# Kernel tuning notes

Hardware: AMD Instinct MI355X
Metric: run time of the kernel (lower is better)

## Reference

```python
import jax, jax.numpy as jnp
import numpy as np

N = 100000       # nodes
E = 3200000      # directed edges (avg_degree ~32)
F_IN = 512
H = 16
C = 7


def setup_inputs() -> dict:
    key = jax.random.key(0)
    k1, k2, k3, k4 = jax.random.split(key, 4)
    x = jax.random.normal(k1, (N, F_IN), dtype=jnp.float32)
    edge_index = jax.random.randint(k2, (2, E), 0, N, dtype=jnp.int32)
    # Glorot-ish init for weights
    W1 = jax.random.normal(k3, (F_IN, H), dtype=jnp.float32) * (1.0 / np.sqrt(F_IN))
    b1 = jnp.zeros((H,), dtype=jnp.float32)
    W2 = jax.random.normal(k4, (H, C), dtype=jnp.float32) * (1.0 / np.sqrt(H))
    b2 = jnp.zeros((C,), dtype=jnp.float32)
    return {"x": x, "edge_index": edge_index, "W1": W1, "b1": b1, "W2": W2, "b2": b2}


def _gcn_prep(edge_index, n):
    # add self-loops (PyG GCNConv default: add_self_loops=True)
    loop = jnp.arange(n, dtype=edge_index.dtype)
    src = jnp.concatenate([edge_index[0], loop])  # [E+N]
    dst = jnp.concatenate([edge_index[1], loop])  # [E+N]
    # symmetric normalization deg^{-1/2} (A+I) deg^{-1/2}; deg over targets
    deg = jax.ops.segment_sum(jnp.ones_like(dst, dtype=jnp.float32), dst, num_segments=n)
    dinv = jax.lax.rsqrt(jnp.maximum(deg, 1.0))  # deg >= 1 due to self-loops
    norm = dinv[src] * dinv[dst]                 # [E+N]
    return src, dst, norm


def _gcn_conv(h, src, dst, norm, W, b, n):
    h = h @ W                                            # [N, out] transform first (small out dim)
    msg = h[src] * norm[:, None]                         # gather + scale, [E+N, out]
    out = jax.ops.segment_sum(msg, dst, num_segments=n)  # scatter-add
    return out + b


def reference(x, edge_index, W1, b1, W2, b2):
    n = x.shape[0]
    src, dst, norm = _gcn_prep(edge_index, n)
    h = _gcn_conv(x, src, dst, norm, W1, b1, n)
    h = jax.nn.relu(h)
    # F.dropout(training=self.training) is identity in eval mode
    h = _gcn_conv(h, src, dst, norm, W2, b2, n)
    return jax.nn.log_softmax(h, axis=1)
```

## Files before the change

### kernel.cpp

```cpp
#include <hip/hip_runtime.h>
#include <math.h>

#define F_IN 512
#define H1 16
#define C_OUT 7
#define BSHIFT 8
#define BNODES 256
#define SRCMASK 0x1FFFFu
#define P3CAP 8960
#define BCAP 8960

__device__ __forceinline__ unsigned bf16pair(float a, float b) {
    unsigned ua = __float_as_uint(a);
    unsigned ub = __float_as_uint(b);
    ua = (ua + 0x7FFFu + ((ua >> 16) & 1u)) >> 16;
    ub = (ub + 0x7FFFu + ((ub >> 16) & 1u)) & 0xFFFF0000u;
    return ua | ub;
}

__global__ __launch_bounds__(1024) void k_zero(int* __restrict__ cur, int B) {
    int t = threadIdx.x;
    if (t < B) cur[t] = 0;
}

__global__ __launch_bounds__(1024) void k_fill_p2(
    const int* __restrict__ src, const int* __restrict__ dst,
    int* __restrict__ cur, unsigned* __restrict__ bedge, int E, int B) {
    __shared__ int lh[1024];
    __shared__ int scan[1024];
    __shared__ int gb[1024];
    __shared__ unsigned lsort[4096];
    __shared__ unsigned short lbk[4096];
    int t = threadIdx.x;
    for (int i = t; i < B; i += 1024) lh[i] = 0;
    __syncthreads();
    int e0 = blockIdx.x * 4096;
    int myb[4], myr[4];
    unsigned myv[4];
#pragma unroll
    for (int k = 0; k < 4; k++) {
        int e = e0 + t + 1024 * k;
        myb[k] = -1;
        if (e < E) {
            int d = dst[e];
            int b = d >> BSHIFT;
            myb[k] = b;
            myv[k] = ((unsigned)(d & (BNODES - 1)) << 17) | (unsigned)src[e];
            myr[k] = atomicAdd(&lh[b], 1);
        }
    }
    __syncthreads();
    int v = (t < B) ? lh[t] : 0;
    scan[t] = v;
    __syncthreads();
    for (int off = 1; off < 1024; off <<= 1) {
        int x = (t >= off) ? scan[t - off] : 0;
        __syncthreads();
        scan[t] += x;
        __syncthreads();
    }
    scan[t] -= v;
    __syncthreads();
    if (t < B && v > 0) gb[t] = t * BCAP + atomicAdd(&cur[t], v);
    __syncthreads();
#pragma unroll
    for (int k = 0; k < 4; k++) {
        if (myb[k] >= 0) {
            int slot = scan[myb[k]] + myr[k];
            lsort[slot] = myv[k];
            lbk[slot] = (unsigned short)myb[k];
        }
    }
    __syncthreads();
    int elim = min(4096, E - e0);
    for (int i = t; i < elim; i += 1024) {
        int b = lbk[i];
        int idx = gb[b] + (i - scan[b]);
        if (idx < (b + 1) * BCAP) bedge[idx] = lsort[i];
    }
}

__global__ __launch_bounds__(256) void k_fill_p3(
    const int* __restrict__ cur, const unsigned* __restrict__ bedge,
    int* __restrict__ csr_src, int* __restrict__ indeg, int* __restrict__ rowptr,
    float* __restrict__ dinv, int n) {
    __shared__ int lh[BNODES];
    __shared__ int off[BNODES];
    __shared__ int lc[BNODES];
    __shared__ int sc[BNODES];
    __shared__ int lsort[P3CAP];
    int t = threadIdx.x;
    int bb = blockIdx.x;
    int nodebase = bb << BSHIFT;
    int gs = bb * BCAP;
    int ge = gs + min(cur[bb], BCAP);
    for (int i = t; i < BNODES; i += 256) { lh[i] = 0; lc[i] = 0; }
    __syncthreads();
    for (int e = gs + t; e < ge; e += 256) {
        unsigned v = bedge[e];
        atomicAdd(&lh[v >> 17], 1);
    }
    __syncthreads();
    int sv = (t < BNODES) ? lh[t] : 0;
    if (t < BNODES) sc[t] = sv;
    __syncthreads();
    for (int o = 1; o < BNODES; o <<= 1) {
        int x = (t < BNODES && t >= o) ? sc[t - o] : 0;
        __syncthreads();
        if (t < BNODES) sc[t] += x;
        __syncthreads();
    }
    if (t < BNODES) off[t] = sc[t] - sv;
    __syncthreads();
    if (t < BNODES) {
        int node = nodebase + t;
        if (node < n) {
            indeg[node] = sv;
            rowptr[node] = gs + off[t];
            dinv[node] = rsqrtf(1.0f + (float)sv);
        }
    }
    for (int e = gs + t; e < ge; e += 256) {
        unsigned v = bedge[e];
        int dl = (int)(v >> 17);
        int rank = atomicAdd(&lc[dl], 1);
        int pos = off[dl] + rank;
        int svv = (int)(v & SRCMASK);
        if (pos < P3CAP) lsort[pos] = svv;
        else csr_src[gs + pos] = svv;
    }
    __syncthreads();
    int lim = min(ge - gs, P3CAP);
    for (int i = t; i < lim; i += 256) csr_src[gs + i] = lsort[i];
}

template<int KH>
__device__ __forceinline__ void gemm1_half(const float* __restrict__ xs,
                                           const float* __restrict__ W1,
                                           int kc, int lrow, float* __restrict__ acc) {
#pragma unroll 4
    for (int k = 0; k < 32; k++) {
        float xv = xs[(KH + k) * 129 + lrow];
        const float* w = W1 + (kc + KH + k) * H1;
#pragma unroll
        for (int c = 0; c < H1; c++) acc[c] = fmaf(xv, w[c], acc[c]);
    }
}

__global__ __launch_bounds__(256) void k_gemm1(
    const float* __restrict__ x, const float* __restrict__ W1,
    const float* __restrict__ dinv, unsigned short* __restrict__ g1, int n) {
    __shared__ float xs[64 * 129];
    const int t = threadIdx.x;
    const int rowbase = blockIdx.x * 128;
    const int lrow = t & 127;
    const int kh = t >> 7;

    float acc[H1];
#pragma unroll
    for (int c = 0; c < H1; c++) acc[c] = 0.0f;

    for (int kc = 0; kc < F_IN; kc += 64) {
        __syncthreads();
#pragma unroll
        for (int jj = 0; jj < 8; jj++) {
            int f = t + 256 * jj;
            int r = f >> 4;
            int kq = f & 15;
            int grow = rowbase + r;
            float4 v = *(const float4*)(x + (size_t)min(grow, n - 1) * F_IN + kc + kq * 4);
            xs[(kq * 4 + 0) * 129 + r] = v.x;
            xs[(kq * 4 + 1) * 129 + r] = v.y;
            xs[(kq * 4 + 2) * 129 + r] = v.z;
            xs[(kq * 4 + 3) * 129 + r] = v.w;
        }
        __syncthreads();
        if (kh == 0) gemm1_half<0>(xs, W1, kc, lrow, acc);
        else         gemm1_half<32>(xs, W1, kc, lrow, acc);
    }
    __syncthreads();
    float* red = xs;
    if (kh == 1) {
#pragma unroll
        for (int c = 0; c < H1; c++) red[lrow * H1 + c] = acc[c];
    }
    __syncthreads();
    if (kh == 0) {
        int grow = rowbase + lrow;
        if (grow < n) {
            float d = dinv[grow];
            float o[H1];
#pragma unroll
            for (int c = 0; c < H1; c++) o[c] = (acc[c] + red[lrow * H1 + c]) * d;
            unsigned pk[8];
#pragma unroll
            for (int k = 0; k < 8; k++) pk[k] = bf16pair(o[2 * k], o[2 * k + 1]);
            unsigned* gp = (unsigned*)(g1 + (size_t)grow * H1);
            *(uint4*)(gp)     = make_uint4(pk[0], pk[1], pk[2], pk[3]);
            *(uint4*)(gp + 4) = make_uint4(pk[4], pk[5], pk[6], pk[7]);
        }
    }
}

__global__ __launch_bounds__(256) void k_agg1(
    const int* __restrict__ rowptr, const int* __restrict__ indeg,
    const int* __restrict__ csr_src, const unsigned short* __restrict__ g1,
    const float* __restrict__ dinv, const float* __restrict__ b1,
    const float* __restrict__ W2, float* __restrict__ g2, int n) {
    int t = threadIdx.x;
    int node = blockIdx.x * 16 + (t >> 4);
    int l = t & 15;
    int eo = l >> 2;
    int c4 = l & 3;
    if (node >= n) return;

    float w[4][C_OUT];
#pragma unroll
    for (int kk = 0; kk < 4; kk++)
#pragma unroll
        for (int c = 0; c < C_OUT; c++)
            w[kk][c] = W2[(c4 * 4 + kk) * C_OUT + c];
    float4 b1c = *(const float4*)(b1 + c4 * 4);

    int start = rowptr[node];
    int end = start + indeg[node];
    float d = dinv[node];

    float4 s = make_float4(0.f, 0.f, 0.f, 0.f);
    if (eo == 0) {
        uint2 u = *(const uint2*)(g1 + (size_t)node * H1 + c4 * 4);
        s.x = __uint_as_float(u.x << 16);
        s.y = __uint_as_float(u.x & 0xFFFF0000u);
        s.z = __uint_as_float(u.y << 16);
        s.w = __uint_as_float(u.y & 0xFFFF0000u);
    }

    int i = start + eo;
    for (; i + 4 < end; i += 8) {
        int a0 = csr_src[i];
        int a1 = csr_src[i + 4];
        uint2 u0 = *(const uint2*)(g1 + (size_t)a0 * H1 + c4 * 4);
        uint2 u1 = *(const uint2*)(g1 + (size_t)a1 * H1 + c4 * 4);
        s.x += __uint_as_float(u0.x << 16)        + __uint_as_float(u1.x << 16);
        s.y += __uint_as_float(u0.x & 0xFFFF0000u) + __uint_as_float(u1.x & 0xFFFF0000u);
        s.z += __uint_as_float(u0.y << 16)        + __uint_as_float(u1.y << 16);
        s.w += __uint_as_float(u0.y & 0xFFFF0000u) + __uint_as_float(u1.y & 0xFFFF0000u);
    }
    if (i < end) {
        int a = csr_src[i];
        uint2 u = *(const uint2*)(g1 + (size_t)a * H1 + c4 * 4);
        s.x += __uint_as_float(u.x << 16);
        s.y += __uint_as_float(u.x & 0xFFFF0000u);
        s.z += __uint_as_float(u.y << 16);
        s.w += __uint_as_float(u.y & 0xFFFF0000u);
    }

    s.x += __shfl_xor(s.x, 4); s.y += __shfl_xor(s.y, 4);
    s.z += __shfl_xor(s.z, 4); s.w += __shfl_xor(s.w, 4);
    s.x += __shfl_xor(s.x, 8); s.y += __shfl_xor(s.y, 8);
    s.z += __shfl_xor(s.z, 8); s.w += __shfl_xor(s.w, 8);

    float4 r;
    r.x = fmaxf(fmaf(d, s.x, b1c.x), 0.f);
    r.y = fmaxf(fmaf(d, s.y, b1c.y), 0.f);
    r.z = fmaxf(fmaf(d, s.z, b1c.z), 0.f);
    r.w = fmaxf(fmaf(d, s.w, b1c.w), 0.f);

    float p[C_OUT];
#pragma unroll
    for (int c = 0; c < C_OUT; c++) {
        p[c] = r.x * w[0][c];
        p[c] = fmaf(r.y, w[1][c], p[c]);
        p[c] = fmaf(r.z, w[2][c], p[c]);
        p[c] = fmaf(r.w, w[3][c], p[c]);
    }
#pragma unroll
    for (int c = 0; c < C_OUT; c++) {
        p[c] += __shfl_xor(p[c], 1);
        p[c] += __shfl_xor(p[c], 2);
    }

    if (eo == 0 && c4 == 0) {
        float4 o = make_float4(d * p[0], d * p[1], d * p[2], d * p[3]);
        *(float4*)(g2 + (size_t)node * 8) = o;
    }
    if (eo == 0 && c4 == 1) {
        float4 o = make_float4(d * p[4], d * p[5], d * p[6], 0.0f);
        *(float4*)(g2 + (size_t)node * 8 + 4) = o;
    }
}

__global__ __launch_bounds__(256) void k_agg2(
    const int* __restrict__ rowptr, const int* __restrict__ indeg,
    const int* __restrict__ csr_src, const float* __restrict__ g2,
    const float* __restrict__ dinv, const float* __restrict__ b2,
    float* __restrict__ out, int n) {
    __shared__ float ls[32 * C_OUT];
    int t = threadIdx.x;
    int g = t >> 3;
    int node = blockIdx.x * 32 + g;
    int l = t & 7;
    int eo = l >> 1;
    int ch = l & 1;

    float4 s = make_float4(0.f, 0.f, 0.f, 0.f);
    float d = 0.f;
    bool valid = node < n;
    if (valid) {
        int start = rowptr[node];
        int end = start + indeg[node];
        d = dinv[node];
        if (eo == 0) s = *(const float4*)(g2 + (size_t)node * 8 + ch * 4);
        int i = start + eo;
        for (; i + 4 < end; i += 8) {
            int a0 = csr_src[i];
            int a1 = csr_src[i + 4];
            float4 v0 = *(const float4*)(g2 + (size_t)a0 * 8 + ch * 4);
            float4 v1 = *(const float4*)(g2 + (size_t)a1 * 8 + ch * 4);
            s.x += v0.x + v1.x;
            s.y += v0.y + v1.y;
            s.z += v0.z + v1.z;
            s.w += v0.w + v1.w;
        }
        if (i < end) {
            int a = csr_src[i];
            float4 v = *(const float4*)(g2 + (size_t)a * 8 + ch * 4);
            s.x += v.x; s.y += v.y; s.z += v.z; s.w += v.w;
        }
    }
    s.x += __shfl_xor(s.x, 2); s.y += __shfl_xor(s.y, 2);
    s.z += __shfl_xor(s.z, 2); s.w += __shfl_xor(s.w, 2);
    s.x += __shfl_xor(s.x, 4); s.y += __shfl_xor(s.y, 4);
    s.z += __shfl_xor(s.z, 4); s.w += __shfl_xor(s.w, 4);

    float4 val;
    if (ch == 0) {
        float4 bb = *(const float4*)b2;
        val.x = fmaf(d, s.x, bb.x);
        val.y = fmaf(d, s.y, bb.y);
        val.z = fmaf(d, s.z, bb.z);
        val.w = fmaf(d, s.w, bb.w);
    } else {
        val.x = fmaf(d, s.x, b2[4]);
        val.y = fmaf(d, s.y, b2[5]);
        val.z = fmaf(d, s.z, b2[6]);
        val.w = 0.f;
    }
    float m = fmaxf(fmaxf(val.x, val.y), val.z);
    if (ch == 0) m = fmaxf(m, val.w);
    m = fmaxf(m, __shfl_xor(m, 1));
    float e0 = expf(val.x - m), e1 = expf(val.y - m), e2 = expf(val.z - m);
    float e3 = (ch == 0) ? expf(val.w - m) : 0.f;
    float se = (e0 + e1) + (e2 + e3);
    se += __shfl_xor(se, 1);
    float lg = logf(se) + m;

    if (valid && eo == 0) {
        float* o = ls + g * C_OUT + ch * 4;
        o[0] = val.x - lg;
        o[1] = val.y - lg;
        o[2] = val.z - lg;
        if (ch == 0) o[3] = val.w - lg;
    }
    __syncthreads();
    int nbase = blockIdx.x * 32;
    int nv = (n - nbase < 32 ? n - nbase : 32) * C_OUT;
    if (t < nv) out[(size_t)nbase * C_OUT + t] = ls[t];
}

extern "C" void kernel_launch(void* const* d_in, const int* in_sizes, int n_in,
                              void* d_out, int out_size, void* d_ws, size_t ws_size,
                              hipStream_t stream) {
    const float* x  = (const float*)d_in[0];
    const int* ei   = (const int*)d_in[1];
    const float* W1 = (const float*)d_in[2];
    const float* b1 = (const float*)d_in[3];
    const float* W2 = (const float*)d_in[4];
    const float* b2 = (const float*)d_in[5];
    float* out = (float*)d_out;

    const int n = in_sizes[0] / F_IN;
    const int E = in_sizes[1] / 2;
    const int* src = ei;
    const int* dst = ei + E;

    const int B   = (n + BNODES - 1) >> BSHIFT;
    const int nfb = (E + 4095) >> 12;

    int*   indeg    = (int*)d_ws;
    int*   rowptr   = indeg + n;
    float* dinv     = (float*)(rowptr + n);
    int*   cur      = (int*)(dinv + n);
    unsigned short* g1 = (unsigned short*)(cur + 1024);
    float* g2       = (float*)(g1 + (size_t)n * H1);
    unsigned* bedge = (unsigned*)(g2 + (size_t)8 * n);
    int*   csr_src  = (int*)(bedge + (size_t)B * BCAP);

    k_zero<<<1, 1024, 0, stream>>>(cur, B);
    k_fill_p2<<<nfb, 1024, 0, stream>>>(src, dst, cur, bedge, E, B);
    k_fill_p3<<<B, 256, 0, stream>>>(cur, bedge, csr_src, indeg, rowptr, dinv, n);

    k_gemm1<<<(n + 127) / 128, 256, 0, stream>>>(x, W1, dinv, g1, n);
    k_agg1<<<(n + 15) / 16, 256, 0, stream>>>(rowptr, indeg, csr_src, g1, dinv, b1, W2, g2, n);
    k_agg2<<<(n + 31) / 32, 256, 0, stream>>>(rowptr, indeg, csr_src, g2, dinv, b2, out, n);
}
```

Before: 414.4 us.

## Merge CSR build stages with degree histogram and GEMM via block-range dispatch

Degrees are now computed with global atomics by extra blocks in the bucket-fill kernel. The CSR sort stage and the first-layer GEMM are merged into one launch that splits work by block index, so the GEMM no longer waits for the sort to finish. The zero kernel is replaced by a memset, and the GEMM computes dinv itself from indeg. This removes two launches and serialization between independent stages, at the cost of 3.2M extra global atomics on indeg and a larger shared-memory footprint for the sort blocks.

```diff
diff --git a/kernel.cpp b/kernel.cpp
--- a/kernel.cpp
+++ b/kernel.cpp
@@ -18,20 +18,25 @@
     return ua | ub;
 }
 
-__global__ __launch_bounds__(1024) void k_zero(int* __restrict__ cur, int B) {
-    int t = threadIdx.x;
-    if (t < B) cur[t] = 0;
-}
-
-__global__ __launch_bounds__(1024) void k_fill_p2(
+__global__ __launch_bounds__(1024) void k_p2hist(
     const int* __restrict__ src, const int* __restrict__ dst,
-    int* __restrict__ cur, unsigned* __restrict__ bedge, int E, int B) {
+    int* __restrict__ cur, unsigned* __restrict__ bedge,
+    int* __restrict__ indeg, int E, int B, int nfb) {
     __shared__ int lh[1024];
     __shared__ int scan[1024];
     __shared__ int gb[1024];
     __shared__ unsigned lsort[4096];
     __shared__ unsigned short lbk[4096];
     int t = threadIdx.x;
+    if ((int)blockIdx.x >= nfb) {
+        int e0 = ((int)blockIdx.x - nfb) * 4096;
+#pragma unroll
+        for (int k = 0; k < 4; k++) {
+            int e = e0 + t + 1024 * k;
+            if (e < E) atomicAdd(&indeg[dst[e]], 1);
+        }
+        return;
+    }
     for (int i = t; i < B; i += 1024) lh[i] = 0;
     __syncthreads();
     int e0 = blockIdx.x * 4096;
@@ -80,60 +85,6 @@
     }
 }
 
-__global__ __launch_bounds__(256) void k_fill_p3(
-    const int* __restrict__ cur, const unsigned* __restrict__ bedge,
-    int* __restrict__ csr_src, int* __restrict__ indeg, int* __restrict__ rowptr,
-    float* __restrict__ dinv, int n) {
-    __shared__ int lh[BNODES];
-    __shared__ int off[BNODES];
-    __shared__ int lc[BNODES];
-    __shared__ int sc[BNODES];
-    __shared__ int lsort[P3CAP];
-    int t = threadIdx.x;
-    int bb = blockIdx.x;
-    int nodebase = bb << BSHIFT;
-    int gs = bb * BCAP;
-    int ge = gs + min(cur[bb], BCAP);
-    for (int i = t; i < BNODES; i += 256) { lh[i] = 0; lc[i] = 0; }
-    __syncthreads();
-    for (int e = gs + t; e < ge; e += 256) {
-        unsigned v = bedge[e];
-        atomicAdd(&lh[v >> 17], 1);
-    }
-    __syncthreads();
-    int sv = (t < BNODES) ? lh[t] : 0;
-    if (t < BNODES) sc[t] = sv;
-    __syncthreads();
-    for (int o = 1; o < BNODES; o <<= 1) {
-        int x = (t < BNODES && t >= o) ? sc[t - o] : 0;
-        __syncthreads();
-        if (t < BNODES) sc[t] += x;
-        __syncthreads();
-    }
-    if (t < BNODES) off[t] = sc[t] - sv;
-    __syncthreads();
-    if (t < BNODES) {
-        int node = nodebase + t;
-        if (node < n) {
-            indeg[node] = sv;
-            rowptr[node] = gs + off[t];
-            dinv[node] = rsqrtf(1.0f + (float)sv);
-        }
-    }
-    for (int e = gs + t; e < ge; e += 256) {
-        unsigned v = bedge[e];
-        int dl = (int)(v >> 17);
-        int rank = atomicAdd(&lc[dl], 1);
-        int pos = off[dl] + rank;
-        int svv = (int)(v & SRCMASK);
-        if (pos < P3CAP) lsort[pos] = svv;
-        else csr_src[gs + pos] = svv;
-    }
-    __syncthreads();
-    int lim = min(ge - gs, P3CAP);
-    for (int i = t; i < lim; i += 256) csr_src[gs + i] = lsort[i];
-}
-
 template<int KH>
 __device__ __forceinline__ void gemm1_half(const float* __restrict__ xs,
                                            const float* __restrict__ W1,
@@ -147,12 +98,62 @@
     }
 }
 
-__global__ __launch_bounds__(256) void k_gemm1(
+__global__ __launch_bounds__(256) void k_p3gemm1(
+    const int* __restrict__ cur, const unsigned* __restrict__ bedge,
+    int* __restrict__ csr_src, int* __restrict__ rowptr,
     const float* __restrict__ x, const float* __restrict__ W1,
-    const float* __restrict__ dinv, unsigned short* __restrict__ g1, int n) {
-    __shared__ float xs[64 * 129];
-    const int t = threadIdx.x;
-    const int rowbase = blockIdx.x * 128;
+    const int* __restrict__ indeg, float* __restrict__ dinv,
+    unsigned short* __restrict__ g1, int n, int B) {
+    __shared__ __align__(16) unsigned char smem[40960];
+    int t = threadIdx.x;
+    if ((int)blockIdx.x < B) {
+        int* lh    = (int*)smem;
+        int* off   = lh + BNODES;
+        int* lc    = off + BNODES;
+        int* sc    = lc + BNODES;
+        int* lsort = sc + BNODES;
+        int bb = blockIdx.x;
+        int gs = bb * BCAP;
+        int ge = gs + min(cur[bb], BCAP);
+        int nodebase = bb << BSHIFT;
+        for (int i = t; i < BNODES; i += 256) { lh[i] = 0; lc[i] = 0; }
+        __syncthreads();
+        for (int e = gs + t; e < ge; e += 256) {
+            unsigned v = bedge[e];
+            atomicAdd(&lh[v >> 17], 1);
+        }
+        __syncthreads();
+        int sv = (t < BNODES) ? lh[t] : 0;
+        if (t < BNODES) sc[t] = sv;
+        __syncthreads();
+        for (int o = 1; o < BNODES; o <<= 1) {
+            int xq = (t < BNODES && t >= o) ? sc[t - o] : 0;
+            __syncthreads();
+            if (t < BNODES) sc[t] += xq;
+            __syncthreads();
+        }
+        if (t < BNODES) off[t] = sc[t] - sv;
+        __syncthreads();
+        if (t < BNODES) {
+            int node = nodebase + t;
+            if (node < n) rowptr[node] = gs + off[t];
+        }
+        for (int e = gs + t; e < ge; e += 256) {
+            unsigned v = bedge[e];
+            int dl = (int)(v >> 17);
+            int rank = atomicAdd(&lc[dl], 1);
+            int pos = off[dl] + rank;
+            int svv = (int)(v & SRCMASK);
+            if (pos < P3CAP) lsort[pos] = svv;
+            else csr_src[gs + pos] = svv;
+        }
+        __syncthreads();
+        int lim = min(ge - gs, P3CAP);
+        for (int i = t; i < lim; i += 256) csr_src[gs + i] = lsort[i];
+        return;
+    }
+    float* xs = (float*)smem;
+    const int rowbase = ((int)blockIdx.x - B) * 128;
     const int lrow = t & 127;
     const int kh = t >> 7;
 
@@ -188,7 +189,8 @@
     if (kh == 0) {
         int grow = rowbase + lrow;
         if (grow < n) {
-            float d = dinv[grow];
+            float d = rsqrtf(1.0f + (float)indeg[grow]);
+            dinv[grow] = d;
             float o[H1];
 #pragma unroll
             for (int c = 0; c < H1; c++) o[c] = (acc[c] + red[lrow * H1 + c]) * d;
@@ -386,21 +388,21 @@
 
     const int B   = (n + BNODES - 1) >> BSHIFT;
     const int nfb = (E + 4095) >> 12;
+    const int ngb = (n + 127) / 128;
 
     int*   indeg    = (int*)d_ws;
-    int*   rowptr   = indeg + n;
+    int*   cur      = indeg + n;
+    int*   rowptr   = cur + 1024;
     float* dinv     = (float*)(rowptr + n);
-    int*   cur      = (int*)(dinv + n);
-    unsigned short* g1 = (unsigned short*)(cur + 1024);
+    unsigned short* g1 = (unsigned short*)(dinv + n);
     float* g2       = (float*)(g1 + (size_t)n * H1);
     unsigned* bedge = (unsigned*)(g2 + (size_t)8 * n);
     int*   csr_src  = (int*)(bedge + (size_t)B * BCAP);
 
-    k_zero<<<1, 1024, 0, stream>>>(cur, B);
-    k_fill_p2<<<nfb, 1024, 0, stream>>>(src, dst, cur, bedge, E, B);
-    k_fill_p3<<<B, 256, 0, stream>>>(cur, bedge, csr_src, indeg, rowptr, dinv, n);
-
-    k_gemm1<<<(n + 127) / 128, 256, 0, stream>>>(x, W1, dinv, g1, n);
+    hipMemsetAsync(indeg, 0, ((size_t)n + 1024) * sizeof(int), stream);
+    k_p2hist<<<nfb * 2, 1024, 0, stream>>>(src, dst, cur, bedge, indeg, E, B, nfb);
+    k_p3gemm1<<<B + ngb, 256, 0, stream>>>(cur, bedge, csr_src, rowptr,
+                                           x, W1, indeg, dinv, g1, n, B);
     k_agg1<<<(n + 15) / 16, 256, 0, stream>>>(rowptr, indeg, csr_src, g1, dinv, b1, W2, g2, n);
     k_agg2<<<(n + 31) / 32, 256, 0, stream>>>(rowptr, indeg, csr_src, g2, dinv, b2, out, n);
 }
```

Result: slower. 529.4 us (+27.8%).
